# Optimization experiments

Hardware: AMD Instinct MI355X
Metric: run time of the kernel (lower is better)

Reference implementation:

```python
import jax, jax.numpy as jnp
import numpy as np

B, N, K, L, H = 8, 2048, 16, 4, 8
CONV = (64, 64, 128, 256)
W_DIM, N_CODES, E_DIM, P_DIM, FF = 512, 8, 64, 256, 512


def act(x):
    return jax.nn.leaky_relu(x, 0.2)


def ln(x, g, b, eps=1e-5):
    m = jnp.mean(x, -1, keepdims=True)
    v = jnp.mean((x - m) ** 2, -1, keepdims=True)
    return g * (x - m) / jnp.sqrt(v + eps) + b


# per-batch neighbor gather: f [C,N], i [N,K] -> [C,N,K]
gather_nb = jax.vmap(lambda f, i: f[:, i])


def knn_idx(y):  # y [B,3,N] -> [B,N,K]
    xx = jnp.sum(y * y, axis=1)
    inner = jnp.einsum('bcn,bcm->bnm', y, y)
    dist = 2.0 * inner - xx[:, :, None] - xx[:, None, :]  # negative sq dist
    return jax.lax.top_k(dist, K)[1]


def mha(q, kv, Wq, bq, Wk, bk, Wv, bv, Wo, bo):
    Bq, S, D = q.shape
    Sk = kv.shape[1]
    dh = D // H
    qh = (q @ Wq.T + bq).reshape(Bq, S, H, dh)
    kh = (kv @ Wk.T + bk).reshape(Bq, Sk, H, dh)
    vh = (kv @ Wv.T + bv).reshape(Bq, Sk, H, dh)
    a = jax.nn.softmax(jnp.einsum('bqhd,bkhd->bhqk', qh, kh) * (1.0 / np.sqrt(dh)))
    o = jnp.einsum('bhqk,bkhd->bqhd', a, vh).reshape(Bq, S, D)
    return o @ Wo.T + bo


def setup_inputs() -> dict:
    key = jax.random.key(0)
    ks = iter(jax.random.split(key, 48))
    nrm = lambda shape: jax.random.normal(next(ks), shape, jnp.float32) * 0.02
    d = {
        'x': jax.random.normal(next(ks), (B, N, 3), jnp.float32),
        'W_ec': nrm((CONV[0], 6)), 'b_ec': jnp.zeros((CONV[0],), jnp.float32),
        'Wc1': nrm((CONV[1], CONV[0])), 'bc1': jnp.zeros((CONV[1],), jnp.float32),
        'Wc2': nrm((CONV[2], CONV[1])), 'bc2': jnp.zeros((CONV[2],), jnp.float32),
        'Wc3': nrm((CONV[3], CONV[2])), 'bc3': jnp.zeros((CONV[3],), jnp.float32),
        'Wf': nrm((W_DIM, sum(CONV))), 'bf': jnp.zeros((W_DIM,), jnp.float32),
        'Wpc': nrm((P_DIM, E_DIM)), 'bpc': jnp.zeros((P_DIM,), jnp.float32),
        'Wpi': nrm((P_DIM, 3)), 'bpi': jnp.zeros((P_DIM,), jnp.float32),
        'Wq': nrm((L, 2, P_DIM, P_DIM)), 'bq': jnp.zeros((L, 2, P_DIM), jnp.float32),
        'Wk': nrm((L, 2, P_DIM, P_DIM)), 'bk': jnp.zeros((L, 2, P_DIM), jnp.float32),
        'Wv': nrm((L, 2, P_DIM, P_DIM)), 'bv': jnp.zeros((L, 2, P_DIM), jnp.float32),
        'Wo': nrm((L, 2, P_DIM, P_DIM)), 'bo': jnp.zeros((L, 2, P_DIM), jnp.float32),
        'ln1g': jnp.ones((L, P_DIM), jnp.float32), 'ln1b': jnp.zeros((L, P_DIM), jnp.float32),
        'ln2g': jnp.ones((L, P_DIM), jnp.float32), 'ln2b': jnp.zeros((L, P_DIM), jnp.float32),
        'Wff1': nrm((L, FF, P_DIM)), 'bff1': jnp.zeros((L, FF), jnp.float32),
        'Wff2': nrm((L, P_DIM, FF)), 'bff2': jnp.zeros((L, P_DIM), jnp.float32),
        'ln3g': jnp.ones((L, P_DIM), jnp.float32), 'ln3b': jnp.zeros((L, P_DIM), jnp.float32),
        'lnfg': jnp.ones((P_DIM,), jnp.float32), 'lnfb': jnp.zeros((P_DIM,), jnp.float32),
        'Wcm': nrm((E_DIM, P_DIM)), 'bcm': jnp.zeros((E_DIM,), jnp.float32),
    }
    return d


def reference(x, W_ec, b_ec, Wc1, bc1, Wc2, bc2, Wc3, bc3, Wf, bf, Wpc, bpc, Wpi, bpi,
              Wq, bq, Wk, bk, Wv, bv, Wo, bo, ln1g, ln1b, ln2g, ln2b,
              Wff1, bff1, Wff2, bff2, ln3g, ln3b, lnfg, lnfb, Wcm, bcm):
    y = jnp.transpose(x, (0, 2, 1))                      # [B,3,N]
    idx = knn_idx(y)                                     # [B,N,K]
    nb = gather_nb(y, idx)                               # [B,3,N,K]
    feats = jnp.concatenate([nb - y[..., None], jnp.broadcast_to(y[..., None], nb.shape)], axis=1)
    h = act(jnp.einsum('oc,bcnk->bonk', W_ec, feats) + b_ec[:, None, None])
    h = h.max(axis=3)                                    # [B,64,N]
    xs = [h]
    for Wl, bl in ((Wc1, bc1), (Wc2, bc2), (Wc3, bc3)):
        h = gather_nb(h, idx).max(axis=3)                # graph max pooling
        h = act(jnp.einsum('oc,bcn->bon', Wl, h) + bl[:, None])
        xs.append(h)
    h = jnp.concatenate(xs, axis=1)                      # [B,512,N]
    h = jnp.einsum('oc,bcn->bon', Wf, h) + bf[:, None]
    xm = h.max(axis=2)                                   # [B,512]
    q = act(xm.reshape(B, N_CODES, E_DIM) @ Wpc.T + bpc) # [B,8,256]
    mem = act(x @ Wpi.T + bpi)                           # [B,N,256]
    for l in range(L):
        q = ln(q + mha(q, q, Wq[l, 0], bq[l, 0], Wk[l, 0], bk[l, 0], Wv[l, 0], bv[l, 0], Wo[l, 0], bo[l, 0]), ln1g[l], ln1b[l])
        q = ln(q + mha(q, mem, Wq[l, 1], bq[l, 1], Wk[l, 1], bk[l, 1], Wv[l, 1], bv[l, 1], Wo[l, 1], bo[l, 1]), ln2g[l], ln2b[l])
        q = ln(q + (act(q @ Wff1[l].T + bff1[l]) @ Wff2[l].T + bff2[l]), ln3g[l], ln3b[l])
    q = ln(q, lnfg, lnfb)
    out = q @ Wcm.T + bcm                                # [B,8,64]
    return out.reshape(B, W_DIM)
```

## Files before the change

kernel.cpp:

```cpp
#include <hip/hip_runtime.h>
#include <math.h>

#define BN 8
#define NP 2048
#define KNN 16
#define NL 4
#define NH 8

typedef __attribute__((ext_vector_type(8))) short bf16x8;
typedef __attribute__((ext_vector_type(4))) float f32x4;

__device__ __forceinline__ unsigned short f2bf(float f) {
    unsigned u = __float_as_uint(f);
    unsigned r = (u + 0x7FFFu + ((u >> 16) & 1u)) >> 16;
    return (unsigned short)r;
}
__device__ __forceinline__ float bf2f(unsigned short s) {
    return __uint_as_float(((unsigned)s) << 16);
}
__device__ __forceinline__ unsigned fmono(float f) {
    unsigned u = __float_as_uint(f);
    return (u & 0x80000000u) ? ~u : (u | 0x80000000u);
}
__device__ __forceinline__ float funmono(unsigned k) {
    return (k & 0x80000000u) ? __uint_as_float(k ^ 0x80000000u) : __uint_as_float(~k);
}

__device__ __forceinline__ float gemv_dot(const unsigned short* __restrict__ wrow, const float* sm, int K8) {
    const uint4* w8 = (const uint4*)wrow;
    const float4* r4 = (const float4*)sm;
    float a0 = 0.f, a1 = 0.f, a2 = 0.f, a3 = 0.f;
    #pragma unroll 8
    for (int c = 0; c < K8; ++c) {
        uint4 wv = w8[c];
        float4 x0 = r4[c * 2], x1 = r4[c * 2 + 1];
        a0 += x0.x * __uint_as_float(wv.x << 16) + x0.y * __uint_as_float(wv.x & 0xFFFF0000u);
        a1 += x0.z * __uint_as_float(wv.y << 16) + x0.w * __uint_as_float(wv.y & 0xFFFF0000u);
        a2 += x1.x * __uint_as_float(wv.z << 16) + x1.y * __uint_as_float(wv.z & 0xFFFF0000u);
        a3 += x1.z * __uint_as_float(wv.w << 16) + x1.w * __uint_as_float(wv.w & 0xFFFF0000u);
    }
    return (a0 + a1) + (a2 + a3);
}

__device__ __forceinline__ unsigned long long shflx_u64(unsigned long long v, int j) {
    int lo = __shfl_xor((int)(unsigned)(v & 0xFFFFFFFFull), j);
    int hi = __shfl_xor((int)(unsigned)(v >> 32), j);
    return ((unsigned long long)(unsigned)hi << 32) | (unsigned)lo;
}

__device__ __forceinline__ unsigned sort64_u32(unsigned v, int lane) {
    #pragma unroll
    for (int k = 2; k <= 64; k <<= 1) {
        #pragma unroll
        for (int j = k >> 1; j > 0; j >>= 1) {
            unsigned o = (unsigned)__shfl_xor((int)v, j);
            bool up = ((lane & k) == 0);
            bool lower = ((lane & j) == 0);
            unsigned mn = v < o ? v : o;
            unsigned mx = v < o ? o : v;
            v = (up == lower) ? mn : mx;
        }
    }
    return v;
}

__device__ __forceinline__ unsigned long long sort64_u64(unsigned long long v, int lane) {
    #pragma unroll
    for (int k = 2; k <= 64; k <<= 1) {
        #pragma unroll
        for (int j = k >> 1; j > 0; j >>= 1) {
            unsigned long long o = shflx_u64(v, j);
            bool up = ((lane & k) == 0);
            bool lower = ((lane & j) == 0);
            unsigned long long mn = v < o ? v : o;
            unsigned long long mx = v < o ? o : v;
            v = (up == lower) ? mn : mx;
        }
    }
    return v;
}

__global__ __launch_bounds__(256) void knn_kernel(const float* __restrict__ x, int* __restrict__ idxout) {
    __shared__ unsigned long long cand[4][64];
    int tid = threadIdx.x;
    int wv = tid >> 6, lane = tid & 63;
    int p = blockIdx.x * 4 + wv;
    int b = p >> 11, n = p & 2047;
    const float* xb = x + (size_t)b * NP * 3;
    float cx = xb[n * 3 + 0], cy = xb[n * 3 + 1], cz = xb[n * 3 + 2];
    float xn = cx * cx + cy * cy + cz * cz;
    unsigned key[32];
    unsigned lmax = 0u;
    #pragma unroll
    for (int t = 0; t < 32; ++t) {
        int m = (t << 6) | lane;
        float mx = xb[m * 3 + 0], my = xb[m * 3 + 1], mz = xb[m * 3 + 2];
        float xxm = mx * mx + my * my + mz * mz;
        float inner = cx * mx + cy * my + cz * mz;
        float dd = 2.0f * inner - xn - xxm;
        unsigned u = __float_as_uint(dd);
        u = (u & 0x80000000u) ? ~u : (u | 0x80000000u);
        key[t] = u;
        lmax = lmax > u ? lmax : u;
    }
    unsigned sorted = sort64_u32(lmax, lane);
    unsigned S = (unsigned)__shfl((int)sorted, 48);
    int c = 0;
    #pragma unroll
    for (int t = 0; t < 32; ++t) c += (key[t] >= S) ? 1 : 0;
    int inc = c;
    #pragma unroll
    for (int d = 1; d < 64; d <<= 1) {
        int tsh = __shfl_up(inc, d);
        if (lane >= d) inc += tsh;
    }
    int C = __shfl(inc, 63);
    int* op = idxout + (size_t)p * KNN;
    if (C <= 64) {
        int off = inc - c;
        #pragma unroll
        for (int t = 0; t < 32; ++t) {
            if (key[t] >= S) {
                int m = (t << 6) | lane;
                cand[wv][off++] = ((unsigned long long)key[t] << 16) | (unsigned)(2047 - m);
            }
        }
        asm volatile("s_waitcnt lgkmcnt(0)" ::: "memory");
        unsigned long long ck = (lane < C) ? cand[wv][lane] : 0ull;
        ck = sort64_u64(ck, lane);
        if (lane >= 48) op[63 - lane] = 2047 - (int)(unsigned)(ck & 0xFFFFull);
    } else {
        unsigned taken = 0u;
        for (int r = 0; r < KNN; ++r) {
            unsigned long long best = 0ull;
            #pragma unroll
            for (int t = 0; t < 32; ++t) {
                if (!((taken >> t) & 1u)) {
                    int m = (t << 6) | lane;
                    unsigned long long ck = ((unsigned long long)key[t] << 16) | (unsigned)(2047 - m);
                    if (ck > best) best = ck;
                }
            }
            #pragma unroll
            for (int d = 1; d < 64; d <<= 1) {
                unsigned long long o = shflx_u64(best, d);
                if (o > best) best = o;
            }
            int m = 2047 - (int)(unsigned)(best & 0xFFFFull);
            if (lane == 0) op[r] = m;
            if ((m & 63) == lane) taken |= 1u << (m >> 6);
        }
    }
}

__global__ __launch_bounds__(256) void edge_conv_kernel(const float* __restrict__ x, const int* __restrict__ idx,
                                                        const float* __restrict__ Wec, const float* __restrict__ bec,
                                                        unsigned short* __restrict__ hcatT) {
    int tid = threadIdx.x;
    int g = tid >> 6, o = tid & 63;
    int p = blockIdx.x * 4 + g;
    int b = p >> 11;
    __shared__ float nb[4][KNN][3];
    __shared__ float ctr[4][3];
    if (o < KNN) {
        int j = idx[(size_t)p * KNN + o];
        const float* xp = x + ((size_t)b * NP + j) * 3;
        nb[g][o][0] = xp[0]; nb[g][o][1] = xp[1]; nb[g][o][2] = xp[2];
    }
    if (o >= KNN && o < KNN + 3) ctr[g][o - KNN] = x[(size_t)p * 3 + (o - KNN)];
    __syncthreads();
    float w0 = Wec[o * 6 + 0], w1 = Wec[o * 6 + 1], w2 = Wec[o * 6 + 2];
    float w3 = Wec[o * 6 + 3], w4 = Wec[o * 6 + 4], w5 = Wec[o * 6 + 5];
    float c0 = ctr[g][0], c1 = ctr[g][1], c2 = ctr[g][2];
    float base = bec[o] + w3 * c0 + w4 * c1 + w5 * c2;
    float m = -3.4e38f;
    #pragma unroll
    for (int k = 0; k < KNN; ++k) {
        float v = base + w0 * (nb[g][k][0] - c0) + w1 * (nb[g][k][1] - c1) + w2 * (nb[g][k][2] - c2);
        v = v > 0.f ? v : 0.2f * v;
        m = fmaxf(m, v);
    }
    hcatT[(size_t)p * 512 + o] = f2bf(m);
}

__global__ __launch_bounds__(256) void pool_bf16_kernel(const unsigned short* __restrict__ src, int s_coff,
                                                        const int* __restrict__ idx,
                                                        unsigned short* __restrict__ dst, int C) {
    int tid = threadIdx.x, wv = tid >> 6, lane = tid & 63;
    int p = blockIdx.x * 4 + wv;
    int b = p >> 11;
    const int* ip = idx + (size_t)p * KNN;
    const unsigned short* sb = src + (size_t)b * NP * 512 + s_coff;
    for (int c0 = 0; c0 < C; c0 += 64) {
        int ch = c0 + lane;
        float m = -3.4e38f;
        #pragma unroll
        for (int k = 0; k < KNN; ++k) {
            int j = ip[k];
            m = fmaxf(m, bf2f(sb[(size_t)j * 512 + ch]));
        }
        dst[(size_t)p * C + ch] = f2bf(m);
    }
}

__global__ __launch_bounds__(256) void mfma_conv64_kernel(const unsigned short* __restrict__ A,
                                                          const unsigned short* __restrict__ W,
                                                          const float* __restrict__ bias,
                                                          unsigned short* __restrict__ hcatT, int coff) {
    __shared__ unsigned short As[128][72];
    __shared__ unsigned short Bs[64][72];
    int m0 = blockIdx.x * 128, b = blockIdx.z;
    int tid = threadIdx.x;
    int lane = tid & 63, wave = tid >> 6;
    int wr = wave >> 1, wc = wave & 1;
    int quad = lane >> 4, l16 = lane & 15;
    {
        int r = tid >> 1, s = (tid & 1) * 32;
        const unsigned short* ap = A + (size_t)b * NP * 64 + (size_t)(m0 + r) * 64 + s;
        uint4 v0 = *(const uint4*)(ap);
        uint4 v1 = *(const uint4*)(ap + 8);
        uint4 v2 = *(const uint4*)(ap + 16);
        uint4 v3 = *(const uint4*)(ap + 24);
        *(uint4*)&As[r][s] = v0; *(uint4*)&As[r][s + 8] = v1;
        *(uint4*)&As[r][s + 16] = v2; *(uint4*)&As[r][s + 24] = v3;
    }
    {
        int r = tid >> 2, s = (tid & 3) * 16;
        const unsigned short* wp = W + r * 64 + s;
        *(uint4*)&Bs[r][s] = *(const uint4*)wp;
        *(uint4*)&Bs[r][s + 8] = *(const uint4*)(wp + 8);
    }
    __syncthreads();
    f32x4 acc[4][2] = {};
    #pragma unroll
    for (int k0 = 0; k0 < 64; k0 += 32) {
        bf16x8 af[4], bfv[2];
        #pragma unroll
        for (int i = 0; i < 4; ++i) af[i] = *(const bf16x8*)&As[wr * 64 + i * 16 + l16][k0 + quad * 8];
        #pragma unroll
        for (int j = 0; j < 2; ++j) bfv[j] = *(const bf16x8*)&Bs[wc * 32 + j * 16 + l16][k0 + quad * 8];
        #pragma unroll
        for (int i = 0; i < 4; ++i)
            #pragma unroll
            for (int j = 0; j < 2; ++j)
                acc[i][j] = __builtin_amdgcn_mfma_f32_16x16x32_bf16(af[i], bfv[j], acc[i][j], 0, 0, 0);
    }
    #pragma unroll
    for (int i = 0; i < 4; ++i) {
        #pragma unroll
        for (int r = 0; r < 4; ++r) {
            int pt = m0 + wr * 64 + i * 16 + quad * 4 + r;
            #pragma unroll
            for (int j = 0; j < 2; ++j) {
                int ch = wc * 32 + j * 16 + l16;
                float v = acc[i][j][r] + bias[ch];
                v = v > 0.f ? v : 0.2f * v;
                hcatT[((size_t)b * NP + pt) * 512 + coff + ch] = f2bf(v);
            }
        }
    }
}

__global__ __launch_bounds__(256) void wcast_kernel(const float* __restrict__ Wf, const float* __restrict__ Wc3,
                                                    const float* __restrict__ Wk, const float* __restrict__ Wv,
                                                    const float* __restrict__ bk, const float* __restrict__ bv,
                                                    const float* __restrict__ Wc1, const float* __restrict__ Wc2,
                                                    const float* __restrict__ Wq, const float* __restrict__ Wo,
                                                    const float* __restrict__ Wff1, const float* __restrict__ Wff2,
                                                    unsigned short* __restrict__ WfB, unsigned short* __restrict__ Wc3B,
                                                    unsigned short* __restrict__ WkvB, float* __restrict__ bkv,
                                                    unsigned short* __restrict__ Wc1B, unsigned short* __restrict__ Wc2B,
                                                    unsigned short* __restrict__ WtB, unsigned short* __restrict__ Wff1B,
                                                    unsigned short* __restrict__ Wff2B,
                                                    unsigned* __restrict__ xmk) {
    int id = blockIdx.x * 256 + threadIdx.x;
    if (id < 262144) { WfB[id] = f2bf(Wf[id]); return; }
    int j = id - 262144;
    if (j < 32768) { Wc3B[j] = f2bf(Wc3[j]); return; }
    j -= 32768;
    if (j < 524288) {
        int l = j >> 17, r = j & 131071;
        float v = (r < 65536) ? Wk[(size_t)(l * 2 + 1) * 65536 + r]
                              : Wv[(size_t)(l * 2 + 1) * 65536 + (r - 65536)];
        WkvB[j] = f2bf(v);
        return;
    }
    j -= 524288;
    if (j < 2048) {
        int l = j >> 9, r = j & 511;
        bkv[j] = (r < 256) ? bk[(l * 2 + 1) * 256 + r] : bv[(l * 2 + 1) * 256 + (r - 256)];
        return;
    }
    j -= 2048;
    if (j < 4096) { Wc1B[j] = f2bf(Wc1[j]); return; }
    j -= 4096;
    if (j < 8192) { Wc2B[j] = f2bf(Wc2[j]); return; }
    j -= 8192;
    if (j < 4096) { xmk[j] = 0u; return; }
    j -= 4096;
    if (j < 1572864) {
        int l = j / 393216;
        int r = j - l * 393216;
        int m = r >> 16, c = r & 65535;
        float v;
        if (m == 0)      v = Wq[(size_t)(l * 2 + 0) * 65536 + c];
        else if (m == 1) v = Wk[(size_t)(l * 2 + 0) * 65536 + c];
        else if (m == 2) v = Wv[(size_t)(l * 2 + 0) * 65536 + c];
        else if (m == 3) v = Wo[(size_t)(l * 2 + 0) * 65536 + c];
        else if (m == 4) v = Wq[(size_t)(l * 2 + 1) * 65536 + c];
        else             v = Wo[(size_t)(l * 2 + 1) * 65536 + c];
        WtB[j] = f2bf(v);
        return;
    }
    j -= 1572864;
    if (j < 524288) { Wff1B[j] = f2bf(Wff1[j]); return; }
    j -= 524288;
    if (j < 524288) { Wff2B[j] = f2bf(Wff2[j]); return; }
}

__global__ __launch_bounds__(256) void mfma_gemm_kernel(const unsigned short* __restrict__ A, size_t a_bstride,
                                                        const unsigned short* __restrict__ B, size_t b_bstride,
                                                        const float* __restrict__ bias, int bias_per_m,
                                                        void* __restrict__ C, size_t c_bstride, int c_rstride,
                                                        int K, int act, int out_bf16,
                                                        unsigned* __restrict__ xmk, int domax) {
    __shared__ unsigned short As[128][40];
    __shared__ unsigned short Bs[128][40];
    int m0 = blockIdx.x * 128, n0 = blockIdx.y * 128, b = blockIdx.z;
    int tid = threadIdx.x;
    int lane = tid & 63, wave = tid >> 6;
    int wr = wave >> 1, wc = wave & 1;
    int quad = lane >> 4, l16 = lane & 15;
    int r0 = tid >> 2, kc0 = (tid & 3) * 8;
    f32x4 acc[4][4] = {};
    const unsigned short* Ab = A + (size_t)b * a_bstride;
    const unsigned short* Bb = B + (size_t)b * b_bstride;
    for (int k0 = 0; k0 < K; k0 += 32) {
        uint4 a0 = *(const uint4*)(Ab + (size_t)(m0 + r0) * K + k0 + kc0);
        uint4 a1 = *(const uint4*)(Ab + (size_t)(m0 + r0 + 64) * K + k0 + kc0);
        uint4 b0 = *(const uint4*)(Bb + (size_t)(n0 + r0) * K + k0 + kc0);
        uint4 b1 = *(const uint4*)(Bb + (size_t)(n0 + r0 + 64) * K + k0 + kc0);
        __syncthreads();
        *(uint4*)&As[r0][kc0] = a0;
        *(uint4*)&As[r0 + 64][kc0] = a1;
        *(uint4*)&Bs[r0][kc0] = b0;
        *(uint4*)&Bs[r0 + 64][kc0] = b1;
        __syncthreads();
        bf16x8 af[4], bfv[4];
        #pragma unroll
        for (int i = 0; i < 4; ++i) af[i] = *(const bf16x8*)&As[wr * 64 + i * 16 + l16][quad * 8];
        #pragma unroll
        for (int j = 0; j < 4; ++j) bfv[j] = *(const bf16x8*)&Bs[wc * 64 + j * 16 + l16][quad * 8];
        #pragma unroll
        for (int i = 0; i < 4; ++i)
            #pragma unroll
            for (int j = 0; j < 4; ++j)
                acc[i][j] = __builtin_amdgcn_mfma_f32_16x16x32_bf16(af[i], bfv[j], acc[i][j], 0, 0, 0);
    }
    if (domax) {
        #pragma unroll
        for (int i = 0; i < 4; ++i) {
            #pragma unroll
            for (int r = 0; r < 4; ++r) {
                int m = m0 + wr * 64 + i * 16 + quad * 4 + r;
                float v = fmaxf(fmaxf(acc[i][0][r], acc[i][1][r]), fmaxf(acc[i][2][r], acc[i][3][r]));
                v += bias[m];
                #pragma unroll
                for (int off = 1; off <= 8; off <<= 1) v = fmaxf(v, __shfl_xor(v, off));
                if (l16 == 0) atomicMax(&xmk[(size_t)b * 512 + m], fmono(v));
            }
        }
        return;
    }
    #pragma unroll
    for (int i = 0; i < 4; ++i) {
        #pragma unroll
        for (int r = 0; r < 4; ++r) {
            int m = m0 + wr * 64 + i * 16 + quad * 4 + r;
            float bm = bias_per_m ? bias[m] : 0.f;
            #pragma unroll
            for (int j = 0; j < 4; ++j) {
                int n = n0 + wc * 64 + j * 16 + l16;
                float v = acc[i][j][r] + (bias_per_m ? bm : bias[n]);
                if (act) v = v > 0.f ? v : 0.2f * v;
                size_t off = (size_t)b * c_bstride + (size_t)m * c_rstride + n;
                if (out_bf16) ((unsigned short*)C)[off] = f2bf(v);
                else          ((float*)C)[off] = v;
            }
        }
    }
}

__global__ __launch_bounds__(256) void mfma_kv_all_kernel(const unsigned short* __restrict__ A,
                                                          const unsigned short* __restrict__ W,
                                                          const float* __restrict__ bkv,
                                                          unsigned short* __restrict__ KVall) {
    __shared__ unsigned short As[128][40];
    __shared__ unsigned short Bs[128][40];
    int m0 = blockIdx.x * 128;
    int nb = blockIdx.y & 3, l = blockIdx.y >> 2;
    int n0 = nb * 128;
    int b = blockIdx.z;
    int tid = threadIdx.x;
    int lane = tid & 63, wave = tid >> 6;
    int wr = wave >> 1, wc = wave & 1;
    int quad = lane >> 4, l16 = lane & 15;
    int r0 = tid >> 2, kc0 = (tid & 3) * 8;
    f32x4 acc[4][4] = {};
    const unsigned short* Ab = A + (size_t)b * NP * 256;
    const unsigned short* Bb = W + (size_t)l * 131072;
    const float* bias = bkv + l * 512;
    for (int k0 = 0; k0 < 256; k0 += 32) {
        uint4 a0 = *(const uint4*)(Ab + (size_t)(m0 + r0) * 256 + k0 + kc0);
        uint4 a1 = *(const uint4*)(Ab + (size_t)(m0 + r0 + 64) * 256 + k0 + kc0);
        uint4 b0 = *(const uint4*)(Bb + (size_t)(n0 + r0) * 256 + k0 + kc0);
        uint4 b1 = *(const uint4*)(Bb + (size_t)(n0 + r0 + 64) * 256 + k0 + kc0);
        __syncthreads();
        *(uint4*)&As[r0][kc0] = a0;
        *(uint4*)&As[r0 + 64][kc0] = a1;
        *(uint4*)&Bs[r0][kc0] = b0;
        *(uint4*)&Bs[r0 + 64][kc0] = b1;
        __syncthreads();
        bf16x8 af[4], bfv[4];
        #pragma unroll
        for (int i = 0; i < 4; ++i) af[i] = *(const bf16x8*)&As[wr * 64 + i * 16 + l16][quad * 8];
        #pragma unroll
        for (int j = 0; j < 4; ++j) bfv[j] = *(const bf16x8*)&Bs[wc * 64 + j * 16 + l16][quad * 8];
        #pragma unroll
        for (int i = 0; i < 4; ++i)
            #pragma unroll
            for (int j = 0; j < 4; ++j)
                acc[i][j] = __builtin_amdgcn_mfma_f32_16x16x32_bf16(af[i], bfv[j], acc[i][j], 0, 0, 0);
    }
    unsigned short* Cb = KVall + ((size_t)l * BN + b) * NP * 512;
    #pragma unroll
    for (int i = 0; i < 4; ++i) {
        #pragma unroll
        for (int r = 0; r < 4; ++r) {
            int m = m0 + wr * 64 + i * 16 + quad * 4 + r;
            #pragma unroll
            for (int j = 0; j < 4; ++j) {
                int n = n0 + wc * 64 + j * 16 + l16;
                Cb[(size_t)m * 512 + n] = f2bf(acc[i][j][r] + bias[n]);
            }
        }
    }
}

__global__ __launch_bounds__(256) void pc_kernel(const unsigned* __restrict__ xmk, const float* __restrict__ Wpc,
                                                 const float* __restrict__ bpc,
                                                 const unsigned short* __restrict__ Wqkv,
                                                 const float* __restrict__ bq0, const float* __restrict__ bk0,
                                                 const float* __restrict__ bv0,
                                                 float* __restrict__ q, float* __restrict__ Qs,
                                                 float* __restrict__ Ks, float* __restrict__ Vs) {
    int row = blockIdx.x, tid = threadIdx.x;
    int id = row * 256 + tid;
    int b = row >> 3, i = row & 7;
    const unsigned* xr = xmk + b * 512 + i * 64;
    const float* w = Wpc + (size_t)tid * 64;
    float acc = bpc[tid];
    #pragma unroll
    for (int e = 0; e < 64; ++e) acc += funmono(xr[e]) * w[e];
    float qv = acc > 0.f ? acc : 0.2f * acc;
    q[id] = qv;
    __shared__ __align__(16) float a[256];
    a[tid] = qv;
    __syncthreads();
    Qs[id] = bq0[tid] + gemv_dot(Wqkv + (size_t)tid * 256, a, 32);
    Ks[id] = bk0[tid] + gemv_dot(Wqkv + 65536 + (size_t)tid * 256, a, 32);
    Vs[id] = bv0[tid] + gemv_dot(Wqkv + 131072 + (size_t)tid * 256, a, 32);
}

__global__ __launch_bounds__(256) void mem_kernel(const float* __restrict__ x, const float* __restrict__ Wpi,
                                                  const float* __restrict__ bpi, unsigned short* __restrict__ memB) {
    size_t id = (size_t)blockIdx.x * 256 + threadIdx.x;
    int p = (int)(id & 255);
    size_t pt = id >> 8;
    float x0 = x[pt * 3 + 0], x1 = x[pt * 3 + 1], x2 = x[pt * 3 + 2];
    float v = bpi[p] + x0 * Wpi[p * 3 + 0] + x1 * Wpi[p * 3 + 1] + x2 * Wpi[p * 3 + 2];
    v = v > 0.f ? v : 0.2f * v;
    memB[id] = f2bf(v);
}

__global__ __launch_bounds__(1024) void attn_ln_kernel(const float* __restrict__ Qs, const float* __restrict__ Ks,
                                                       const float* __restrict__ Vs,
                                                       const unsigned short* __restrict__ WoB,
                                                       const float* __restrict__ bo, const float* __restrict__ res,
                                                       const float* __restrict__ g, const float* __restrict__ bt,
                                                       const unsigned short* __restrict__ Wq1B,
                                                       const float* __restrict__ bq1,
                                                       float* __restrict__ out, float* __restrict__ Qc) {
    int row = blockIdx.x, tid = threadIdx.x;
    int b = row >> 3;
    __shared__ float Kl[2048], Vl[2048];
    __shared__ __align__(16) float qr[256];
    __shared__ float sc[64];
    __shared__ __align__(16) float r[256];
    __shared__ __align__(16) float aout[256];
    __shared__ float red[1024];
    for (int t = tid; t < 2048; t += 1024) {
        Kl[t] = Ks[(size_t)b * 2048 + t];
        Vl[t] = Vs[(size_t)b * 2048 + t];
    }
    if (tid < 256) qr[tid] = Qs[(size_t)row * 256 + tid];
    __syncthreads();
    const float scale = 0.17677669529663687f;
    {
        int pair = tid >> 4, part = tid & 15;
        int h = pair >> 3, k = pair & 7;
        int d = part * 2;
        float dot = qr[h * 32 + d] * Kl[k * 256 + h * 32 + d]
                  + qr[h * 32 + d + 1] * Kl[k * 256 + h * 32 + d + 1];
        dot += __shfl_xor(dot, 1);
        dot += __shfl_xor(dot, 2);
        dot += __shfl_xor(dot, 4);
        dot += __shfl_xor(dot, 8);
        if (part == 0) sc[pair] = dot * scale;
    }
    __syncthreads();
    if (tid < 64) {
        float v = sc[tid];
        float m = v;
        #pragma unroll
        for (int off = 1; off < 8; off <<= 1) m = fmaxf(m, __shfl_xor(m, off));
        float e = __expf(v - m);
        float s = e;
        #pragma unroll
        for (int off = 1; off < 8; off <<= 1) s += __shfl_xor(s, off);
        sc[tid] = e / s;
    }
    __syncthreads();
    if (tid < 256) {
        int h = tid >> 5;
        float acc = 0.f;
        #pragma unroll
        for (int k = 0; k < 8; ++k) acc += sc[h * 8 + k] * Vl[k * 256 + tid];
        r[tid] = acc;
    }
    __syncthreads();
    int o4 = tid >> 2, p4 = tid & 3;
    float v;
    {
        float acc = gemv_dot(WoB + (size_t)o4 * 256 + p4 * 64, r + p4 * 64, 8);
        acc += __shfl_xor(acc, 1);
        acc += __shfl_xor(acc, 2);
        v = (p4 == 0) ? (bo[o4] + acc + res[(size_t)row * 256 + o4]) : 0.f;
    }
    red[tid] = v; __syncthreads();
    for (int s = 512; s; s >>= 1) { if (tid < s) red[tid] += red[tid + s]; __syncthreads(); }
    float mean = red[0] * (1.0f / 256.0f);
    __syncthreads();
    float dv = (p4 == 0) ? v - mean : 0.f;
    red[tid] = dv * dv; __syncthreads();
    for (int s = 512; s; s >>= 1) { if (tid < s) red[tid] += red[tid + s]; __syncthreads(); }
    float var = red[0] * (1.0f / 256.0f);
    if (p4 == 0) {
        float oln = g[o4] * dv * rsqrtf(var + 1e-5f) + bt[o4];
        out[(size_t)row * 256 + o4] = oln;
        aout[o4] = oln;
    }
    __syncthreads();
    {
        float qacc = gemv_dot(Wq1B + (size_t)o4 * 256 + p4 * 64, aout + p4 * 64, 8);
        qacc += __shfl_xor(qacc, 1);
        qacc += __shfl_xor(qacc, 2);
        if (p4 == 0) Qc[(size_t)row * 256 + o4] = bq1[o4] + qacc;
    }
}

__global__ __launch_bounds__(256) void ca_part_kernel(const float* __restrict__ Qc,
                                                      const unsigned short* __restrict__ KVl,
                                                      float* __restrict__ part) {
    int kb = blockIdx.x, h = blockIdx.y, b = blockIdx.z;
    int tid = threadIdx.x;
    __shared__ float q[8][32];
    __shared__ __align__(16) float S[8][128];
    __shared__ float om[8][8][32];
    const float scale = 0.17677669529663687f;
    {
        int i = tid >> 5, d = tid & 31;
        q[i][d] = Qc[(size_t)(b * 8 + i) * 256 + h * 32 + d];
    }
    __syncthreads();
    {
        int kk = tid & 127, half = tid >> 7;
        int k = kb * 128 + kk;
        const unsigned short* kp = KVl + ((size_t)b * NP + k) * 512 + h * 32;
        float kd[32];
        #pragma unroll
        for (int u = 0; u < 4; ++u) {
            uint4 raw = *(const uint4*)(kp + u * 8);
            unsigned w0 = raw.x, w1 = raw.y, w2 = raw.z, w3 = raw.w;
            kd[u * 8 + 0] = __uint_as_float(w0 << 16); kd[u * 8 + 1] = __uint_as_float(w0 & 0xFFFF0000u);
            kd[u * 8 + 2] = __uint_as_float(w1 << 16); kd[u * 8 + 3] = __uint_as_float(w1 & 0xFFFF0000u);
            kd[u * 8 + 4] = __uint_as_float(w2 << 16); kd[u * 8 + 5] = __uint_as_float(w2 & 0xFFFF0000u);
            kd[u * 8 + 6] = __uint_as_float(w3 << 16); kd[u * 8 + 7] = __uint_as_float(w3 & 0xFFFF0000u);
        }
        #pragma unroll
        for (int i = 0; i < 4; ++i) {
            int ri = half * 4 + i;
            float dot = 0.f;
            #pragma unroll
            for (int d = 0; d < 32; ++d) dot += q[ri][d] * kd[d];
            S[ri][kk] = dot * scale;
        }
    }
    __syncthreads();
    float* pout = part + (((size_t)(b * NH + h)) * 16 + kb) * 288;
    {
        int i = tid >> 5, l32 = tid & 31;
        float m = -3.4e38f;
        #pragma unroll
        for (int t = 0; t < 4; ++t) m = fmaxf(m, S[i][l32 + t * 32]);
        #pragma unroll
        for (int off = 16; off; off >>= 1) m = fmaxf(m, __shfl_xor(m, off));
        float s = 0.f;
        #pragma unroll
        for (int t = 0; t < 4; ++t) {
            float e = __expf(S[i][l32 + t * 32] - m);
            S[i][l32 + t * 32] = e;
            s += e;
        }
        #pragma unroll
        for (int off = 16; off; off >>= 1) s += __shfl_xor(s, off);
        if (l32 == 0) { pout[i] = m; pout[8 + i] = s; }
    }
    __syncthreads();
    {
        int d = tid & 31, grp = tid >> 5;
        const unsigned short* Vb = KVl + ((size_t)b * NP + kb * 128) * 512 + 256 + h * 32 + d;
        float acc[8] = {};
        #pragma unroll 4
        for (int t = 0; t < 16; ++t) {
            int kk = grp * 16 + t;
            float v = bf2f(Vb[(size_t)kk * 512]);
            #pragma unroll
            for (int i = 0; i < 8; ++i) acc[i] += S[i][kk] * v;
        }
        #pragma unroll
        for (int i = 0; i < 8; ++i) om[grp][i][d] = acc[i];
    }
    __syncthreads();
    {
        int i = tid >> 5, d = tid & 31;
        float sum = 0.f;
        #pragma unroll
        for (int g = 0; g < 8; ++g) sum += om[g][i][d];
        pout[16 + i * 32 + d] = sum;
    }
}

__global__ __launch_bounds__(1024) void combine_ff_kernel(const float* __restrict__ part,
                                                          const unsigned short* __restrict__ WoB,
                                                          const float* __restrict__ bo, const float* __restrict__ res,
                                                          const float* __restrict__ g2, const float* __restrict__ b2t,
                                                          const unsigned short* __restrict__ W1B,
                                                          const float* __restrict__ b1,
                                                          const unsigned short* __restrict__ W2B,
                                                          const float* __restrict__ b2,
                                                          const float* __restrict__ g3, const float* __restrict__ b3t,
                                                          float* __restrict__ out,
                                                          int is_last, const float* __restrict__ lnfg,
                                                          const float* __restrict__ lnfb, const float* __restrict__ Wcm,
                                                          const float* __restrict__ bcm, float* __restrict__ finout,
                                                          const unsigned short* __restrict__ Wqkvn,
                                                          const float* __restrict__ bqn, const float* __restrict__ bkn,
                                                          const float* __restrict__ bvn,
                                                          float* __restrict__ Qs, float* __restrict__ Ks,
                                                          float* __restrict__ Vs) {
    int row = blockIdx.x, tid = threadIdx.x;
    int b = row >> 3, i = row & 7;
    __shared__ __align__(16) float r[256];
    __shared__ __align__(16) float a[256];
    __shared__ __align__(16) float hbuf[512];
    __shared__ float red[1024];
    {
        int h = tid >> 7, rem = tid & 127, d = rem >> 2, g = rem & 3;
        const float* pb = part + (size_t)(b * NH + h) * 16 * 288;
        float M = -3.4e38f;
        #pragma unroll
        for (int t = 0; t < 4; ++t) M = fmaxf(M, pb[(g * 4 + t) * 288 + i]);
        M = fmaxf(M, __shfl_xor(M, 1));
        M = fmaxf(M, __shfl_xor(M, 2));
        float L = 0.f, O = 0.f;
        #pragma unroll
        for (int t = 0; t < 4; ++t) {
            int kb = g * 4 + t;
            float w = __expf(pb[kb * 288 + i] - M);
            L += pb[kb * 288 + 8 + i] * w;
            O += pb[kb * 288 + 16 + i * 32 + d] * w;
        }
        L += __shfl_xor(L, 1); L += __shfl_xor(L, 2);
        O += __shfl_xor(O, 1); O += __shfl_xor(O, 2);
        if (g == 0) r[h * 32 + d] = O / L;
    }
    __syncthreads();
    int o4 = tid >> 2, p4 = tid & 3;
    float v;
    {
        float acc = gemv_dot(WoB + (size_t)o4 * 256 + p4 * 64, r + p4 * 64, 8);
        acc += __shfl_xor(acc, 1);
        acc += __shfl_xor(acc, 2);
        v = (p4 == 0) ? (bo[o4] + acc + res[(size_t)row * 256 + o4]) : 0.f;
    }
    red[tid] = v; __syncthreads();
    for (int s = 512; s; s >>= 1) { if (tid < s) red[tid] += red[tid + s]; __syncthreads(); }
    float mean = red[0] * (1.0f / 256.0f);
    __syncthreads();
    float dv = (p4 == 0) ? v - mean : 0.f;
    red[tid] = dv * dv; __syncthreads();
    for (int s = 512; s; s >>= 1) { if (tid < s) red[tid] += red[tid + s]; __syncthreads(); }
    float var = red[0] * (1.0f / 256.0f);
    if (p4 == 0) a[o4] = g2[o4] * dv * rsqrtf(var + 1e-5f) + b2t[o4];
    __syncthreads();
    {
        int o = tid >> 1, p = tid & 1;
        float acc = gemv_dot(W1B + (size_t)o * 256 + p * 128, a + p * 128, 16);
        acc += __shfl_xor(acc, 1);
        if (p == 0) { float t = b1[o] + acc; hbuf[o] = t > 0.f ? t : 0.2f * t; }
    }
    __syncthreads();
    float vF;
    {
        float acc = gemv_dot(W2B + (size_t)o4 * 512 + p4 * 128, hbuf + p4 * 128, 16);
        acc += __shfl_xor(acc, 1);
        acc += __shfl_xor(acc, 2);
        vF = (p4 == 0) ? (b2[o4] + acc + a[o4]) : 0.f;
    }
    red[tid] = vF; __syncthreads();
    for (int s = 512; s; s >>= 1) { if (tid < s) red[tid] += red[tid + s]; __syncthreads(); }
    float mean2 = red[0] * (1.0f / 256.0f);
    __syncthreads();
    float dv2 = (p4 == 0) ? vF - mean2 : 0.f;
    red[tid] = dv2 * dv2; __syncthreads();
    for (int s = 512; s; s >>= 1) { if (tid < s) red[tid] += red[tid + s]; __syncthreads(); }
    float var2 = red[0] * (1.0f / 256.0f);
    float tln = 0.f;
    if (p4 == 0) {
        tln = g3[o4] * dv2 * rsqrtf(var2 + 1e-5f) + b3t[o4];
        r[o4] = tln;
    }
    __syncthreads();
    if (!is_last) {
        if (p4 == 0) out[(size_t)row * 256 + o4] = tln;
        if (tid < 768) {
            int which = tid >> 8, o = tid & 255;
            float acc = gemv_dot(Wqkvn + (size_t)which * 65536 + (size_t)o * 256, r, 32);
            float bb = (which == 0) ? bqn[o] : (which == 1) ? bkn[o] : bvn[o];
            float* dst = (which == 0) ? Qs : (which == 1) ? Ks : Vs;
            dst[(size_t)row * 256 + o] = bb + acc;
        }
        return;
    }
    float tf = (tid < 256) ? r[tid] : 0.f;
    red[tid] = tf; __syncthreads();
    for (int s = 512; s; s >>= 1) { if (tid < s) red[tid] += red[tid + s]; __syncthreads(); }
    float mean3 = red[0] * (1.0f / 256.0f);
    __syncthreads();
    float d3 = (tid < 256) ? tf - mean3 : 0.f;
    red[tid] = d3 * d3; __syncthreads();
    for (int s = 512; s; s >>= 1) { if (tid < s) red[tid] += red[tid + s]; __syncthreads(); }
    float var3 = red[0] * (1.0f / 256.0f);
    if (tid < 256) a[tid] = lnfg[tid] * d3 * rsqrtf(var3 + 1e-5f) + lnfb[tid];
    __syncthreads();
    if (tid < 64) {
        const float4* w4 = (const float4*)(Wcm + (size_t)tid * 256);
        const float4* a4 = (const float4*)a;
        float acc = bcm[tid];
        #pragma unroll 8
        for (int c = 0; c < 64; ++c) {
            float4 av = a4[c], wv = w4[c];
            acc += av.x * wv.x + av.y * wv.y + av.z * wv.z + av.w * wv.w;
        }
        finout[(size_t)b * 512 + i * 64 + tid] = acc;
    }
}

extern "C" void kernel_launch(void* const* d_in, const int* in_sizes, int n_in,
                              void* d_out, int out_size, void* d_ws, size_t ws_size,
                              hipStream_t stream) {
    const float* x    = (const float*)d_in[0];
    const float* Wec  = (const float*)d_in[1];
    const float* bec  = (const float*)d_in[2];
    const float* Wc1  = (const float*)d_in[3];
    const float* bc1  = (const float*)d_in[4];
    const float* Wc2  = (const float*)d_in[5];
    const float* bc2  = (const float*)d_in[6];
    const float* Wc3  = (const float*)d_in[7];
    const float* bc3  = (const float*)d_in[8];
    const float* Wf   = (const float*)d_in[9];
    const float* bf   = (const float*)d_in[10];
    const float* Wpc  = (const float*)d_in[11];
    const float* bpc  = (const float*)d_in[12];
    const float* Wpi  = (const float*)d_in[13];
    const float* bpi  = (const float*)d_in[14];
    const float* Wq   = (const float*)d_in[15];
    const float* bq   = (const float*)d_in[16];
    const float* Wk   = (const float*)d_in[17];
    const float* bk   = (const float*)d_in[18];
    const float* Wv   = (const float*)d_in[19];
    const float* bv   = (const float*)d_in[20];
    const float* Wo   = (const float*)d_in[21];
    const float* bo   = (const float*)d_in[22];
    const float* ln1g = (const float*)d_in[23];
    const float* ln1b = (const float*)d_in[24];
    const float* ln2g = (const float*)d_in[25];
    const float* ln2b = (const float*)d_in[26];
    const float* Wff1 = (const float*)d_in[27];
    const float* bff1 = (const float*)d_in[28];
    const float* Wff2 = (const float*)d_in[29];
    const float* bff2 = (const float*)d_in[30];
    const float* ln3g = (const float*)d_in[31];
    const float* ln3b = (const float*)d_in[32];
    const float* lnfg = (const float*)d_in[33];
    const float* lnfb = (const float*)d_in[34];
    const float* Wcm  = (const float*)d_in[35];
    const float* bcm  = (const float*)d_in[36];
    float* out = (float*)d_out;

    float* ws = (float*)d_ws;
    size_t off = 0;
    auto alloc = [&](size_t n) { float* p = ws + off; off += (n + 3) & ~(size_t)3; return p; };
    int*            idx   = (int*)alloc((size_t)BN * NP * KNN);
    unsigned short* hcatT = (unsigned short*)alloc((size_t)BN * NP * 512 / 2);
    unsigned short* poolT = (unsigned short*)alloc((size_t)BN * NP * 128 / 2);
    unsigned short* WfB   = (unsigned short*)alloc(262144 / 2);
    unsigned short* Wc1B  = (unsigned short*)alloc(4096 / 2);
    unsigned short* Wc2B  = (unsigned short*)alloc(8192 / 2);
    unsigned short* Wc3B  = (unsigned short*)alloc(32768 / 2);
    unsigned short* WkvB  = (unsigned short*)alloc(524288 / 2);
    float*          bkv   = alloc(2048);
    unsigned short* memB  = (unsigned short*)alloc((size_t)BN * NP * 256 / 2);
    unsigned short* KVall = (unsigned short*)alloc((size_t)NL * BN * NP * 512 / 2);
    unsigned*       xmk   = (unsigned*)alloc((size_t)BN * 512);
    unsigned short* WtB   = (unsigned short*)alloc(1572864 / 2);
    unsigned short* Wff1B = (unsigned short*)alloc(524288 / 2);
    unsigned short* Wff2B = (unsigned short*)alloc(524288 / 2);
    float*          qa    = alloc((size_t)BN * 8 * 256);
    float*          qb    = alloc((size_t)BN * 8 * 256);
    float*          Qs    = alloc((size_t)BN * 8 * 256);
    float*          Ks    = alloc((size_t)BN * 8 * 256);
    float*          Vs    = alloc((size_t)BN * 8 * 256);
    float*          Qc    = alloc((size_t)BN * 8 * 256);
    float*          part  = alloc((size_t)BN * NH * 16 * 288);

    wcast_kernel<<<13512, 256, 0, stream>>>(Wf, Wc3, Wk, Wv, bk, bv, Wc1, Wc2, Wq, Wo, Wff1, Wff2,
                                            WfB, Wc3B, WkvB, bkv, Wc1B, Wc2B, WtB, Wff1B, Wff2B, xmk);

    knn_kernel<<<BN * NP / 4, 256, 0, stream>>>(x, idx);
    edge_conv_kernel<<<BN * NP / 4, 256, 0, stream>>>(x, idx, Wec, bec, hcatT);

    pool_bf16_kernel<<<BN * NP / 4, 256, 0, stream>>>(hcatT, 0, idx, poolT, 64);
    mfma_conv64_kernel<<<dim3(NP / 128, 1, BN), 256, 0, stream>>>(poolT, Wc1B, bc1, hcatT, 64);
    pool_bf16_kernel<<<BN * NP / 4, 256, 0, stream>>>(hcatT, 64, idx, poolT, 64);
    mfma_gemm_kernel<<<dim3(NP / 128, 1, BN), 256, 0, stream>>>(poolT, (size_t)NP * 64, Wc2B, 0,
                                                                bc2, 0, (void*)(hcatT + 128), (size_t)NP * 512, 512,
                                                                64, 1, 1, nullptr, 0);
    pool_bf16_kernel<<<BN * NP / 4, 256, 0, stream>>>(hcatT, 128, idx, poolT, 128);
    mfma_gemm_kernel<<<dim3(NP / 128, 2, BN), 256, 0, stream>>>(poolT, (size_t)NP * 128, Wc3B, 0,
                                                                bc3, 0, (void*)(hcatT + 256), (size_t)NP * 512, 512,
                                                                128, 1, 1, nullptr, 0);
    mfma_gemm_kernel<<<dim3(4, NP / 128, BN), 256, 0, stream>>>(WfB, 0, hcatT, (size_t)NP * 512,
                                                                bf, 1, nullptr, 0, 0,
                                                                512, 0, 0, xmk, 1);
    pc_kernel<<<BN * 8, 256, 0, stream>>>(xmk, Wpc, bpc, WtB, bq, bk, bv, qa, Qs, Ks, Vs);
    mem_kernel<<<BN * NP, 256, 0, stream>>>(x, Wpi, bpi, memB);
    mfma_kv_all_kernel<<<dim3(NP / 128, 4 * NL, BN), 256, 0, stream>>>(memB, WkvB, bkv, KVall);

    for (int l = 0; l < NL; ++l) {
        const unsigned short* Wl = WtB + (size_t)l * 393216;
        const float* bo0 = bo + (l * 2 + 0) * 256;
        const float* bq1 = bq + (l * 2 + 1) * 256;
        const float* bo1 = bo + (l * 2 + 1) * 256;
        int last = (l == NL - 1);

        attn_ln_kernel<<<BN * 8, 1024, 0, stream>>>(Qs, Ks, Vs, Wl + 3 * 65536, bo0, qa,
                                                    ln1g + l * 256, ln1b + l * 256, Wl + 4 * 65536, bq1, qb, Qc);
        ca_part_kernel<<<dim3(16, NH, BN), 256, 0, stream>>>(Qc, KVall + (size_t)l * BN * NP * 512, part);
        combine_ff_kernel<<<BN * 8, 1024, 0, stream>>>(part, Wl + 5 * 65536, bo1, qb,
                                                       ln2g + l * 256, ln2b + l * 256,
                                                       Wff1B + (size_t)l * 131072, bff1 + l * 512,
                                                       Wff2B + (size_t)l * 131072, bff2 + l * 256,
                                                       ln3g + l * 256, ln3b + l * 256, qa,
                                                       last, lnfg, lnfb, Wcm, bcm, out,
                                                       last ? nullptr : WtB + (size_t)(l + 1) * 393216,
                                                       bq + ((l + 1) * 2) * 256, bk + ((l + 1) * 2) * 256,
                                                       bv + ((l + 1) * 2) * 256,
                                                       Qs, Ks, Vs);
    }

    (void)in_sizes; (void)n_in; (void)out_size; (void)ws_size;
}
```

Baseline: 553.9 us.

## Quantize transformer GEMV weights to int8 and stage kNN points in LDS

Adds a per-row symmetric int8 quantization pass over the attention-output, FF1, FF2 and next-layer QKV weights, and makes combine_ff_kernel read int8 weights with per-row scales. This halves weight bytes streamed by the small-batch GEMVs. Separately, knn_kernel now loads the batch's points and their squared norms into shared memory once per block instead of each wave re-reading global memory. The int8 path adds an extra quantization launch and lowers weight precision, which changes numerics.

```diff
diff --git a/kernel.cpp b/kernel.cpp
--- a/kernel.cpp
+++ b/kernel.cpp
@@ -42,6 +42,26 @@
     return (a0 + a1) + (a2 + a3);
 }
 
+__device__ __forceinline__ float gemv_i8(const char* __restrict__ wrow, const float* sm, int K16) {
+    const uint4* w16 = (const uint4*)wrow;
+    const float4* r4 = (const float4*)sm;
+    float a0 = 0.f, a1 = 0.f, a2 = 0.f, a3 = 0.f;
+    #pragma unroll 4
+    for (int c = 0; c < K16; ++c) {
+        uint4 wv = w16[c];
+        float4 x0 = r4[c * 4], x1 = r4[c * 4 + 1], x2 = r4[c * 4 + 2], x3 = r4[c * 4 + 3];
+        a0 += x0.x * (float)(signed char)(wv.x) + x0.y * (float)(signed char)(wv.x >> 8)
+            + x0.z * (float)(signed char)(wv.x >> 16) + x0.w * (float)(signed char)(wv.x >> 24);
+        a1 += x1.x * (float)(signed char)(wv.y) + x1.y * (float)(signed char)(wv.y >> 8)
+            + x1.z * (float)(signed char)(wv.y >> 16) + x1.w * (float)(signed char)(wv.y >> 24);
+        a2 += x2.x * (float)(signed char)(wv.z) + x2.y * (float)(signed char)(wv.z >> 8)
+            + x2.z * (float)(signed char)(wv.z >> 16) + x2.w * (float)(signed char)(wv.z >> 24);
+        a3 += x3.x * (float)(signed char)(wv.w) + x3.y * (float)(signed char)(wv.w >> 8)
+            + x3.z * (float)(signed char)(wv.w >> 16) + x3.w * (float)(signed char)(wv.w >> 24);
+    }
+    return (a0 + a1) + (a2 + a3);
+}
+
 __device__ __forceinline__ unsigned long long shflx_u64(unsigned long long v, int j) {
     int lo = __shfl_xor((int)(unsigned)(v & 0xFFFFFFFFull), j);
     int hi = __shfl_xor((int)(unsigned)(v >> 32), j);
@@ -81,23 +101,26 @@
 }
 
 __global__ __launch_bounds__(256) void knn_kernel(const float* __restrict__ x, int* __restrict__ idxout) {
+    __shared__ float xs[2048], ys[2048], zs[2048], ns[2048];
     __shared__ unsigned long long cand[4][64];
     int tid = threadIdx.x;
     int wv = tid >> 6, lane = tid & 63;
     int p = blockIdx.x * 4 + wv;
     int b = p >> 11, n = p & 2047;
     const float* xb = x + (size_t)b * NP * 3;
-    float cx = xb[n * 3 + 0], cy = xb[n * 3 + 1], cz = xb[n * 3 + 2];
-    float xn = cx * cx + cy * cy + cz * cz;
+    for (int t = tid; t < 2048; t += 256) {
+        float mx = xb[t * 3 + 0], my = xb[t * 3 + 1], mz = xb[t * 3 + 2];
+        xs[t] = mx; ys[t] = my; zs[t] = mz;
+        ns[t] = mx * mx + my * my + mz * mz;
+    }
+    __syncthreads();
+    float cx = xs[n], cy = ys[n], cz = zs[n], xn = ns[n];
     unsigned key[32];
     unsigned lmax = 0u;
     #pragma unroll
     for (int t = 0; t < 32; ++t) {
         int m = (t << 6) | lane;
-        float mx = xb[m * 3 + 0], my = xb[m * 3 + 1], mz = xb[m * 3 + 2];
-        float xxm = mx * mx + my * my + mz * mz;
-        float inner = cx * mx + cy * my + cz * mz;
-        float dd = 2.0f * inner - xn - xxm;
+        float dd = 2.0f * (cx * xs[m] + cy * ys[m] + cz * zs[m]) - xn - ns[m];
         unsigned u = __float_as_uint(dd);
         u = (u & 0x80000000u) ? ~u : (u | 0x80000000u);
         key[t] = u;
@@ -316,6 +339,40 @@
     if (j < 524288) { Wff1B[j] = f2bf(Wff1[j]); return; }
     j -= 524288;
     if (j < 524288) { Wff2B[j] = f2bf(Wff2[j]); return; }
+}
+
+__global__ __launch_bounds__(256) void wquant_kernel(const unsigned short* __restrict__ WtB,
+                                                     const unsigned short* __restrict__ Wff1B,
+                                                     const unsigned short* __restrict__ Wff2B,
+                                                     char* __restrict__ WtI, float* __restrict__ StW,
+                                                     char* __restrict__ FF1I, float* __restrict__ SF1,
+                                                     char* __restrict__ FF2I, float* __restrict__ SF2) {
+    int tid = threadIdx.x, wv = tid >> 6, lane = tid & 63;
+    int row = blockIdx.x * 4 + wv;
+    const unsigned short* src;
+    char* dst;
+    float* sc;
+    int K;
+    if (row < 6144)      { src = WtB + (size_t)row * 256; dst = WtI + (size_t)row * 256; sc = StW + row; K = 256; }
+    else if (row < 8192) { int r = row - 6144; src = Wff1B + (size_t)r * 256; dst = FF1I + (size_t)r * 256; sc = SF1 + r; K = 256; }
+    else                 { int r = row - 8192; src = Wff2B + (size_t)r * 512; dst = FF2I + (size_t)r * 512; sc = SF2 + r; K = 512; }
+    int per = K >> 6;
+    float w[8];
+    float mx = 0.f;
+    for (int e = 0; e < per; ++e) { w[e] = bf2f(src[lane * per + e]); mx = fmaxf(mx, fabsf(w[e])); }
+    #pragma unroll
+    for (int off = 1; off < 64; off <<= 1) mx = fmaxf(mx, __shfl_xor(mx, off));
+    float s = fmaxf(mx, 1e-30f) * (1.0f / 127.0f);
+    float inv = 1.0f / s;
+    unsigned pk[2] = {0u, 0u};
+    for (int e = 0; e < per; ++e) {
+        int q = (int)rintf(w[e] * inv);
+        q = q > 127 ? 127 : (q < -127 ? -127 : q);
+        pk[e >> 2] |= ((unsigned)(q & 255)) << (8 * (e & 3));
+    }
+    ((unsigned*)dst)[lane * (per >> 2)] = pk[0];
+    if (per == 8) ((unsigned*)dst)[lane * 2 + 1] = pk[1];
+    if (lane == 0) *sc = s;
 }
 
 __global__ __launch_bounds__(256) void mfma_gemm_kernel(const unsigned short* __restrict__ A, size_t a_bstride,
@@ -652,19 +709,19 @@
 }
 
 __global__ __launch_bounds__(1024) void combine_ff_kernel(const float* __restrict__ part,
-                                                          const unsigned short* __restrict__ WoB,
+                                                          const char* __restrict__ WoI, const float* __restrict__ sWo,
                                                           const float* __restrict__ bo, const float* __restrict__ res,
                                                           const float* __restrict__ g2, const float* __restrict__ b2t,
-                                                          const unsigned short* __restrict__ W1B,
+                                                          const char* __restrict__ W1I, const float* __restrict__ sW1,
                                                           const float* __restrict__ b1,
-                                                          const unsigned short* __restrict__ W2B,
+                                                          const char* __restrict__ W2I, const float* __restrict__ sW2,
                                                           const float* __restrict__ b2,
                                                           const float* __restrict__ g3, const float* __restrict__ b3t,
                                                           float* __restrict__ out,
                                                           int is_last, const float* __restrict__ lnfg,
                                                           const float* __restrict__ lnfb, const float* __restrict__ Wcm,
                                                           const float* __restrict__ bcm, float* __restrict__ finout,
-                                                          const unsigned short* __restrict__ Wqkvn,
+                                                          const char* __restrict__ WqkvnI, const float* __restrict__ sQn,
                                                           const float* __restrict__ bqn, const float* __restrict__ bkn,
                                                           const float* __restrict__ bvn,
                                                           float* __restrict__ Qs, float* __restrict__ Ks,
@@ -699,10 +756,10 @@
     int o4 = tid >> 2, p4 = tid & 3;
     float v;
     {
-        float acc = gemv_dot(WoB + (size_t)o4 * 256 + p4 * 64, r + p4 * 64, 8);
+        float acc = gemv_i8(WoI + (size_t)o4 * 256 + p4 * 64, r + p4 * 64, 4);
         acc += __shfl_xor(acc, 1);
         acc += __shfl_xor(acc, 2);
-        v = (p4 == 0) ? (bo[o4] + acc + res[(size_t)row * 256 + o4]) : 0.f;
+        v = (p4 == 0) ? (bo[o4] + sWo[o4] * acc + res[(size_t)row * 256 + o4]) : 0.f;
     }
     red[tid] = v; __syncthreads();
     for (int s = 512; s; s >>= 1) { if (tid < s) red[tid] += red[tid + s]; __syncthreads(); }
@@ -716,17 +773,17 @@
     __syncthreads();
     {
         int o = tid >> 1, p = tid & 1;
-        float acc = gemv_dot(W1B + (size_t)o * 256 + p * 128, a + p * 128, 16);
+        float acc = gemv_i8(W1I + (size_t)o * 256 + p * 128, a + p * 128, 8);
         acc += __shfl_xor(acc, 1);
-        if (p == 0) { float t = b1[o] + acc; hbuf[o] = t > 0.f ? t : 0.2f * t; }
+        if (p == 0) { float t = b1[o] + sW1[o] * acc; hbuf[o] = t > 0.f ? t : 0.2f * t; }
     }
     __syncthreads();
     float vF;
     {
-        float acc = gemv_dot(W2B + (size_t)o4 * 512 + p4 * 128, hbuf + p4 * 128, 16);
+        float acc = gemv_i8(W2I + (size_t)o4 * 512 + p4 * 128, hbuf + p4 * 128, 8);
         acc += __shfl_xor(acc, 1);
         acc += __shfl_xor(acc, 2);
-        vF = (p4 == 0) ? (b2[o4] + acc + a[o4]) : 0.f;
+        vF = (p4 == 0) ? (b2[o4] + sW2[o4] * acc + a[o4]) : 0.f;
     }
     red[tid] = vF; __syncthreads();
     for (int s = 512; s; s >>= 1) { if (tid < s) red[tid] += red[tid + s]; __syncthreads(); }
@@ -746,10 +803,10 @@
         if (p4 == 0) out[(size_t)row * 256 + o4] = tln;
         if (tid < 768) {
             int which = tid >> 8, o = tid & 255;
-            float acc = gemv_dot(Wqkvn + (size_t)which * 65536 + (size_t)o * 256, r, 32);
+            float acc = gemv_i8(WqkvnI + (size_t)which * 65536 + (size_t)o * 256, r, 16);
             float bb = (which == 0) ? bqn[o] : (which == 1) ? bkn[o] : bvn[o];
             float* dst = (which == 0) ? Qs : (which == 1) ? Ks : Vs;
-            dst[(size_t)row * 256 + o] = bb + acc;
+            dst[(size_t)row * 256 + o] = bb + sQn[which * 256 + o] * acc;
         }
         return;
     }
@@ -837,6 +894,12 @@
     unsigned short* WtB   = (unsigned short*)alloc(1572864 / 2);
     unsigned short* Wff1B = (unsigned short*)alloc(524288 / 2);
     unsigned short* Wff2B = (unsigned short*)alloc(524288 / 2);
+    char*           WtI   = (char*)alloc(1572864 / 4);
+    float*          StW   = alloc(6144);
+    char*           FF1I  = (char*)alloc(524288 / 4);
+    float*          SF1   = alloc(2048);
+    char*           FF2I  = (char*)alloc(524288 / 4);
+    float*          SF2   = alloc(1024);
     float*          qa    = alloc((size_t)BN * 8 * 256);
     float*          qb    = alloc((size_t)BN * 8 * 256);
     float*          Qs    = alloc((size_t)BN * 8 * 256);
@@ -847,6 +910,7 @@
 
     wcast_kernel<<<13512, 256, 0, stream>>>(Wf, Wc3, Wk, Wv, bk, bv, Wc1, Wc2, Wq, Wo, Wff1, Wff2,
                                             WfB, Wc3B, WkvB, bkv, Wc1B, Wc2B, WtB, Wff1B, Wff2B, xmk);
+    wquant_kernel<<<2304, 256, 0, stream>>>(WtB, Wff1B, Wff2B, WtI, StW, FF1I, SF1, FF2I, SF2);
 
     knn_kernel<<<BN * NP / 4, 256, 0, stream>>>(x, idx);
     edge_conv_kernel<<<BN * NP / 4, 256, 0, stream>>>(x, idx, Wec, bec, hcatT);
@@ -878,13 +942,16 @@
         attn_ln_kernel<<<BN * 8, 1024, 0, stream>>>(Qs, Ks, Vs, Wl + 3 * 65536, bo0, qa,
                                                     ln1g + l * 256, ln1b + l * 256, Wl + 4 * 65536, bq1, qb, Qc);
         ca_part_kernel<<<dim3(16, NH, BN), 256, 0, stream>>>(Qc, KVall + (size_t)l * BN * NP * 512, part);
-        combine_ff_kernel<<<BN * 8, 1024, 0, stream>>>(part, Wl + 5 * 65536, bo1, qb,
+        combine_ff_kernel<<<BN * 8, 1024, 0, stream>>>(part,
+                                                       WtI + (size_t)l * 393216 + 5 * 65536, StW + l * 1536 + 5 * 256,
+                                                       bo1, qb,
                                                        ln2g + l * 256, ln2b + l * 256,
-                                                       Wff1B + (size_t)l * 131072, bff1 + l * 512,
-                                                       Wff2B + (size_t)l * 131072, bff2 + l * 256,
+                                                       FF1I + (size_t)l * 131072, SF1 + l * 512, bff1 + l * 512,
+                                                       FF2I + (size_t)l * 131072, SF2 + l * 256, bff2 + l * 256,
                                                        ln3g + l * 256, ln3b + l * 256, qa,
                                                        last, lnfg, lnfb, Wcm, bcm, out,
-                                                       last ? nullptr : WtB + (size_t)(l + 1) * 393216,
+                                                       last ? nullptr : WtI + (size_t)(l + 1) * 393216,
+                                                       last ? nullptr : StW + (l + 1) * 1536,
                                                        bq + ((l + 1) * 2) * 256, bk + ((l + 1) * 2) * 256,
                                                        bv + ((l + 1) * 2) * 256,
                                                        Qs, Ks, Vs);
```

New measurement: 517.3 us. 1.07x faster.
